# Kernel tuning notes

Hardware: AMD Instinct MI355X
Metric: run time of the kernel (lower is better)

Reference implementation:

```python
import jax, jax.numpy as jnp
import numpy as np

B, N0, N1, FD, L, H = 4, 256, 256, 128, 3, 1
NG = N0 + N1            # nodes per graph
N = B * NG              # total nodes
EPS_BN = 1e-5
EPS_SM = 1e-16


def _build_edges():
    def perm_edges(n, off):
        idx = np.arange(n)
        a = np.repeat(idx, n); b = np.tile(idx, n)
        m = a != b
        return np.stack([a[m], b[m]]) + off
    e_intra = np.concatenate([perm_edges(N0, 0), perm_edges(N1, N0)], axis=1)
    a = np.arange(N0); b = np.arange(N0, N0 + N1)
    cross1 = np.stack([np.repeat(a, N1), np.tile(b, N0)])
    cross2 = np.stack([np.repeat(b, N0), np.tile(a, N1)])
    eg = np.concatenate([e_intra, cross1, cross2], axis=1)
    tg = np.concatenate([np.zeros(e_intra.shape[1], np.int32),
                         np.ones(cross1.shape[1] + cross2.shape[1], np.int32)])
    ei = np.concatenate([eg + g * NG for g in range(B)], axis=1).astype(np.int32)
    et = np.tile(tg, B).astype(np.int32)
    return jnp.asarray(ei), jnp.asarray(et)


def setup_inputs() -> dict:
    key = jax.random.key(0)
    ks = jax.random.split(key, 8)
    edge_index, edge_type = _build_edges()
    return {
        'desc0': jax.random.normal(ks[0], (B, FD, N0), jnp.float32),
        'desc1': jax.random.normal(ks[1], (B, FD, N1), jnp.float32),
        'W': jax.random.normal(ks[2], (L, 2, FD, H * FD), jnp.float32) * (1.0 / np.sqrt(FD)),
        'q': jax.random.normal(ks[3], (L, H * FD, H), jnp.float32) * 0.1,
        'k': jax.random.normal(ks[4], (L, H * FD, H), jnp.float32) * 0.1,
        'conv_b': jnp.zeros((L, FD), jnp.float32),
        'lin_W': jax.random.normal(ks[5], (L, FD, 2 * FD), jnp.float32) * (1.0 / np.sqrt(2 * FD)),
        'lin_b': jnp.zeros((L, FD), jnp.float32),
        'gamma': jnp.ones((L, FD), jnp.float32),
        'beta': jnp.zeros((L, FD), jnp.float32),
        'edge_index': edge_index,
        'edge_type': edge_type,
    }


def _forward(desc0, desc1, W, q, k, conv_b, lin_W, lin_b, gamma, beta, edge_index, edge_type):
    # x: [B, NG, FD] -> flattened batch graph [N, FD]
    x = jnp.concatenate([desc0, desc1], axis=2)        # [B, FD, NG]
    x = jnp.transpose(x, (0, 2, 1)).reshape(N, FD)
    src, dst = edge_index[0], edge_index[1]
    nlayers = W.shape[0]
    heads = q.shape[2]
    for l in range(nlayers):
        # relation-specific node projections (equiv to per-edge bmm with weight[edge_type])
        proj = jnp.einsum('nf,rfo->nro', x, W[l])       # [N, 2, H*FD]
        out_i = proj[dst, edge_type]                    # [E, H*FD]
        out_j = proj[src, edge_type]                    # [E, H*FD]
        alpha = jax.nn.leaky_relu(out_i @ q[l] + out_j @ k[l], 0.2)  # [E, H]
        # softmax over incoming edges of each destination node (across-relation)
        amax = jax.ops.segment_max(alpha, dst, num_segments=N)
        ex = jnp.exp(alpha - amax[dst])
        denom = jax.ops.segment_sum(ex, dst, num_segments=N)
        att = ex / (denom[dst] + EPS_SM)                # [E, H]
        msg = (att[:, :, None] * out_j.reshape(-1, heads, FD)).reshape(-1, heads * FD)
        agg = jax.ops.segment_sum(msg, dst, num_segments=N).reshape(N, heads, FD)
        m1 = jax.nn.relu(agg.mean(axis=1) + conv_b[l])  # concat=False -> mean over heads
        m2 = jnp.concatenate([x, m1], axis=1) @ lin_W[l].T + lin_b[l]
        mu = m2.mean(axis=0)
        var = ((m2 - mu) ** 2).mean(axis=0)             # biased var (BatchNorm training)
        m3 = (m2 - mu) / jnp.sqrt(var + EPS_BN) * gamma[l] + beta[l]
        x = x + m3
    x = x.reshape(B, NG, FD).transpose(0, 2, 1)         # [B, FD, NG]
    return x


def reference(desc0, desc1, W, q, k, conv_b, lin_W, lin_b, gamma, beta, edge_index, edge_type):
    x = _forward(desc0, desc1, W, q, k, conv_b, lin_W, lin_b, gamma, beta, edge_index, edge_type)
    return x[:, :, :N0], x[:, :, N0:]
```

## Files before the change

kernel.cpp:

```cpp
#include <hip/hip_runtime.h>

#define FD  128
#define NN  2048

#define OFF_X     0
#define OFF_QS    262144
#define OFF_KS    266240
#define OFF_SUMS  270336
#define OFF_LWT   276480
#define OFF_M2    374784
#define OFF_QH    636928
#define OFF_KH    637696

__device__ __forceinline__ int swizzle_n0(int bid) {
    int g    = (bid & 7) >> 1;
    int slot = ((bid >> 3) << 1) | (bid & 1);
    return g*512 + slot*4;
}

__device__ __forceinline__ void qsks0(
    const float* __restrict__ W, const float* __restrict__ qv,
    const float* __restrict__ kv, float* __restrict__ ws,
    int n0, int t, const float (*xs)[FD],
    float (*redp)[256], float* red)
{
    int kh = t >> 8, tp = t & 255;
    int rsel = tp >> 7, o = tp & 127;
    const float* Wl = W + ((size_t)rsel*FD)*FD + o;
    float acc[4];
#pragma unroll
    for (int r = 0; r < 4; r++) acc[r] = 0.f;
    int kbase = kh * 64;
#pragma unroll
    for (int kk = 0; kk < 64; kk += 4) {
        int k4 = kbase + kk;
        float w0 = Wl[(k4+0)*FD], w1 = Wl[(k4+1)*FD];
        float w2 = Wl[(k4+2)*FD], w3 = Wl[(k4+3)*FD];
#pragma unroll
        for (int r = 0; r < 4; r++) {
            float4 xq = *(const float4*)&xs[r][k4];
            acc[r] += xq.x*w0 + xq.y*w1 + xq.z*w2 + xq.w*w3;
        }
    }
    if (kh == 1) {
#pragma unroll
        for (int r = 0; r < 4; r++) redp[r][tp] = acc[r];
    }
    __syncthreads();
    if (t < 256) {
#pragma unroll
        for (int r = 0; r < 4; r++) acc[r] += redp[r][tp];
        float qq = qv[o], kq = kv[o];
        int lane = t & 63, w = t >> 6;
#pragma unroll
        for (int r = 0; r < 4; r++) {
            float vq = acc[r]*qq, vk = acc[r]*kq;
            for (int off = 32; off; off >>= 1) {
                vq += __shfl_xor(vq, off, 64);
                vk += __shfl_xor(vk, off, 64);
            }
            if (lane == 0) { red[w*8 + r*2] = vq; red[w*8 + r*2 + 1] = vk; }
        }
    }
    __syncthreads();
    if (t < 16) {
        int r = t & 3, rs = (t >> 2) & 1, wh = t >> 3;
        float v = red[(rs*2)*8 + r*2 + wh] + red[(rs*2 + 1)*8 + r*2 + wh];
        if (wh == 0) ws[OFF_QS + rs*NN + n0 + r] = v;
        else         ws[OFF_KS + rs*NN + n0 + r] = v;
    }
}

__global__ __launch_bounds__(512, 4) void k_pre(
    const float* __restrict__ d0, const float* __restrict__ d1,
    const float* __restrict__ W,  const float* __restrict__ qv,
    const float* __restrict__ kv, const float* __restrict__ linW,
    float* __restrict__ ws)
{
    int bid = blockIdx.x, t = threadIdx.x;
    if (bid >= 512) {
        if (bid < 536) {
            int vb = bid - 512;
#pragma unroll
            for (int i = 0; i < 8; i++) {
                int e = vb*4096 + i*512 + t;
                int l = e >> 15, rem = e & 32767;
                int o = rem >> 8, c = rem & 255;
                ws[OFF_LWT + l*32768 + c*FD + o] = linW[e];
            }
        } else {
            for (int i = t; i < 6144; i += 512) ws[OFF_SUMS + i] = 0.f;
#pragma unroll
            for (int ii = 0; ii < 3; ii++) {
                int e = ii*512 + t;
                int sel = e & 1, idx = e >> 1;
                const float* wrow = W + (size_t)idx*FD;
                int l = idx >> 8;
                const float* vvec = sel ? (kv + l*FD) : (qv + l*FD);
                float acc = 0.f;
                for (int o = 0; o < FD; o++) acc += wrow[o]*vvec[o];
                ws[(sel ? OFF_KH : OFF_QH) + idx] = acc;
            }
        }
        return;
    }
    __shared__ __attribute__((aligned(16))) float xs[4][FD];
    __shared__ float redp[4][256];
    __shared__ float red[32];
    int n0 = swizzle_n0(bid);
    {
        int row = t >> 7, f = t & 127;
        int n = n0 + row, gg = n >> 9, ii = n & 511;
        float v = (ii < 256) ? d0[gg*32768 + f*256 + ii]
                             : d1[gg*32768 + f*256 + (ii - 256)];
        xs[row][f] = v;
        ws[OFF_X + (size_t)n*FD + f] = v;
    }
    __syncthreads();
    qsks0(W, qv, kv, ws, n0, t, xs, redp, red);
}

__global__ __launch_bounds__(512, 4) void k_qs(
    const float* __restrict__ gamma, const float* __restrict__ beta,
    float* __restrict__ ws, int l)
{
    __shared__ float scale[FD], shift[FD];
    __shared__ float red[4][8];
    int bid = blockIdx.x, t = threadIdx.x;
    int lp = l - 1;
    if (t < 128) {
        float s0 = 0.f, s1 = 0.f;
#pragma unroll
        for (int sl = 0; sl < 8; sl++) {
            s0 += ws[OFF_SUMS + lp*2048 + sl*256 + t];
            s1 += ws[OFF_SUMS + lp*2048 + sl*256 + 128 + t];
        }
        float mu  = s0 * (1.f/2048.f);
        float var = s1 * (1.f/2048.f) - mu*mu;
        float rs  = rsqrtf(var + 1e-5f);
        float gm  = gamma[lp*FD + t], bt = beta[lp*FD + t];
        scale[t] = gm * rs;
        shift[t] = bt - mu * gm * rs;
    }
    __syncthreads();
    int n0 = swizzle_n0(bid);
    int row = t >> 7, f = t & 127;
    size_t e = (size_t)(n0 + row)*FD + f;
    float xv = ws[OFF_X + e] + ws[OFF_M2 + e]*scale[f] + shift[f];
    ws[OFF_X + e] = xv;
    float p0 = xv * ws[OFF_QH + l*256 + f];
    float p1 = xv * ws[OFF_QH + l*256 + 128 + f];
    float p2 = xv * ws[OFF_KH + l*256 + f];
    float p3 = xv * ws[OFF_KH + l*256 + 128 + f];
    for (int off = 32; off; off >>= 1) {
        p0 += __shfl_xor(p0, off, 64);
        p1 += __shfl_xor(p1, off, 64);
        p2 += __shfl_xor(p2, off, 64);
        p3 += __shfl_xor(p3, off, 64);
    }
    int lane = t & 63, wh = (t >> 6) & 1;
    if (lane == 0) {
        red[row][wh*4+0] = p0; red[row][wh*4+1] = p1;
        red[row][wh*4+2] = p2; red[row][wh*4+3] = p3;
    }
    __syncthreads();
    if (t < 16) {
        int r = t >> 2, j = t & 3;
        float v = red[r][j] + red[r][4+j];
        int n = n0 + r;
        if      (j == 0) ws[OFF_QS + n] = v;
        else if (j == 1) ws[OFF_QS + NN + n] = v;
        else if (j == 2) ws[OFF_KS + n] = v;
        else             ws[OFF_KS + NN + n] = v;
    }
}

__global__ __launch_bounds__(512, 4) void k_attn(
    const float* __restrict__ Wg,    const float* __restrict__ convb,
    const float* __restrict__ linb,  float* __restrict__ ws, int l)
{
    __shared__ __attribute__((aligned(16))) float att[4*512];
    __shared__ __attribute__((aligned(16))) float redB[8*4*128];
    __shared__ __attribute__((aligned(16))) float hgc[4*256];
    __shared__ float sml[4][2], sls[4][2];
    __shared__ float r1[FD], r2[FD];

    int bid = blockIdx.x, t = threadIdx.x;
    int dstbase = swizzle_n0(bid);
    int g = dstbase >> 9, dloc0 = dstbase & 511;
    int Gd = (dloc0 >= 256) ? 1 : 0;

    {
        int w = t >> 6, p = t & 63;
        int d = w >> 1, h = w & 1;
        int dloc = dloc0 + d;
        float q0 = ws[OFF_QS + dstbase + d];
        float q1 = ws[OFF_QS + NN + dstbase + d];
        float sc[4];
#pragma unroll
        for (int j = 0; j < 4; j++) {
            int s = h*256 + p + j*64;
            int ts = (s < 256) ? Gd : 1 - Gd;
            float a = (ts ? q1 : q0) + ws[OFF_KS + ts*NN + g*512 + s];
            a = a > 0.f ? a : 0.2f*a;
            sc[j] = (s == dloc) ? -1e30f : a;
        }
        float lm = fmaxf(fmaxf(sc[0], sc[1]), fmaxf(sc[2], sc[3]));
        for (int off = 32; off; off >>= 1) lm = fmaxf(lm, __shfl_xor(lm, off, 64));
        float ex[4], lsum = 0.f;
#pragma unroll
        for (int j = 0; j < 4; j++) { ex[j] = __expf(sc[j] - lm); lsum += ex[j]; }
        for (int off = 32; off; off >>= 1) lsum += __shfl_xor(lsum, off, 64);
#pragma unroll
        for (int j = 0; j < 4; j++) att[d*512 + h*256 + p + j*64] = ex[j];
        if (p == 0) { sml[d][h] = lm; sls[d][h] = lsum; }
    }
    __syncthreads();
    {
        int d = t >> 7, s4 = (t & 127) * 4;
        int h = (s4 >= 256) ? 1 : 0;
        float m0 = sml[d][0], m1 = sml[d][1];
        float M = fmaxf(m0, m1);
        float denom = sls[d][0]*__expf(m0 - M) + sls[d][1]*__expf(m1 - M) + 1e-16f;
        float fac = __expf(sml[d][h] - M) / denom;
        float4 a4 = *(float4*)&att[d*512 + s4];
        a4.x *= fac; a4.y *= fac; a4.z *= fac; a4.w *= fac;
        *(float4*)&att[d*512 + s4] = a4;
        if (t < 128) r1[t] = 0.f;
        else if (t < 256) r2[t - 128] = 0.f;
    }
    __syncthreads();

    int f4 = t & 31, sq = t >> 5;
    float acc[4][4];
#pragma unroll
    for (int d2 = 0; d2 < 4; d2++)
#pragma unroll
        for (int j = 0; j < 4; j++) acc[d2][j] = 0.f;
    {
        const float* xp = ws + OFF_X + (size_t)(g*512)*FD + f4*4;
        int s0 = sq * 32;
        float4 bufA[4], bufB[4];
#pragma unroll
        for (int u = 0; u < 4; u++) bufA[u] = *(const float4*)&xp[(size_t)(s0+u)*FD];
#pragma unroll
        for (int ii = 0; ii < 8; ii++) {
            const float4* cur = (ii & 1) ? bufB : bufA;
            float4*       nxt = (ii & 1) ? bufA : bufB;
            if (ii < 7) {
#pragma unroll
                for (int u = 0; u < 4; u++)
                    nxt[u] = *(const float4*)&xp[(size_t)(s0 + (ii+1)*4 + u)*FD];
            }
#pragma unroll
            for (int u = 0; u < 4; u++) {
                int s = s0 + ii*4 + u;
                float4 v = cur[u];
#pragma unroll
                for (int d2 = 0; d2 < 4; d2++) {
                    float b = att[d2*512 + s];
                    acc[d2][0] += b*v.x; acc[d2][1] += b*v.y;
                    acc[d2][2] += b*v.z; acc[d2][3] += b*v.w;
                }
            }
        }
    }
    {
        int slot = (sq & 3) + ((sq >> 3) << 2);
        if (sq & 4) {
#pragma unroll
            for (int d2 = 0; d2 < 4; d2++)
                *(float4*)&redB[(slot*4 + d2)*128 + f4*4] =
                    make_float4(acc[d2][0], acc[d2][1], acc[d2][2], acc[d2][3]);
        }
        __syncthreads();
        if (!(sq & 4)) {
#pragma unroll
            for (int d2 = 0; d2 < 4; d2++) {
                float4 p4 = *(const float4*)&redB[(slot*4 + d2)*128 + f4*4];
                *(float4*)&redB[(slot*4 + d2)*128 + f4*4] =
                    make_float4(acc[d2][0]+p4.x, acc[d2][1]+p4.y, acc[d2][2]+p4.z, acc[d2][3]+p4.w);
            }
        }
        __syncthreads();
    }
    {
        int d2 = t >> 7, f = t & 127;
        float hg0 = redB[(0*4+d2)*128+f] + redB[(1*4+d2)*128+f]
                  + redB[(2*4+d2)*128+f] + redB[(3*4+d2)*128+f];
        float hg1 = redB[(4*4+d2)*128+f] + redB[(5*4+d2)*128+f]
                  + redB[(6*4+d2)*128+f] + redB[(7*4+d2)*128+f];
        hgc[d2*256 + f]       = Gd ? hg1 : hg0;
        hgc[d2*256 + 128 + f] = Gd ? hg0 : hg1;
    }
    __syncthreads();

#pragma unroll
    for (int d2 = 0; d2 < 4; d2++)
#pragma unroll
        for (int j = 0; j < 4; j++) acc[d2][j] = 0.f;
    {
        int rel = sq >> 3;
        const float* wp = Wg + ((size_t)((l*2 + rel)*FD) + (sq & 7)*16)*FD + f4*4;
        int c0 = sq * 16;
        float4 wA[4], wB[4];
#pragma unroll
        for (int u = 0; u < 4; u++) wA[u] = *(const float4*)&wp[(size_t)u*FD];
#pragma unroll
        for (int ii = 0; ii < 4; ii++) {
            const float4* cur = (ii & 1) ? wB : wA;
            float4*       nxt = (ii & 1) ? wA : wB;
            if (ii < 3) {
#pragma unroll
                for (int u = 0; u < 4; u++)
                    nxt[u] = *(const float4*)&wp[(size_t)((ii+1)*4 + u)*FD];
            }
#pragma unroll
            for (int u = 0; u < 4; u++) {
                int c = c0 + ii*4 + u;
                float4 w4 = cur[u];
#pragma unroll
                for (int d2 = 0; d2 < 4; d2++) {
                    float cv = hgc[d2*256 + c];
                    acc[d2][0] += cv*w4.x; acc[d2][1] += cv*w4.y;
                    acc[d2][2] += cv*w4.z; acc[d2][3] += cv*w4.w;
                }
            }
        }
    }
    if (sq >= 8) {
#pragma unroll
        for (int d2 = 0; d2 < 4; d2++)
            *(float4*)&redB[((sq - 8)*4 + d2)*128 + f4*4] =
                make_float4(acc[d2][0], acc[d2][1], acc[d2][2], acc[d2][3]);
    }
    __syncthreads();
    if (sq < 8) {
#pragma unroll
        for (int d2 = 0; d2 < 4; d2++) {
            float4 p4 = *(const float4*)&redB[(sq*4 + d2)*128 + f4*4];
            *(float4*)&redB[(sq*4 + d2)*128 + f4*4] =
                make_float4(acc[d2][0]+p4.x, acc[d2][1]+p4.y, acc[d2][2]+p4.z, acc[d2][3]+p4.w);
        }
    }
    __syncthreads();

    {
        int d2 = t >> 7, f = t & 127;
        float agg = 0.f;
#pragma unroll
        for (int cc = 0; cc < 8; cc++) agg += redB[(cc*4 + d2)*128 + f];
        float m1v = fmaxf(agg + convb[l*FD + f], 0.f);
        hgc[d2*256 + 128 + f] = m1v;
        hgc[d2*256 + f] = ws[OFF_X + (size_t)(dstbase + d2)*FD + f];
    }
    __syncthreads();

#pragma unroll
    for (int d2 = 0; d2 < 4; d2++)
#pragma unroll
        for (int j = 0; j < 4; j++) acc[d2][j] = 0.f;
    {
        const float* lwt = ws + OFF_LWT + l*32768 + f4*4;
        int c0 = sq * 16;
        float4 wA[4], wB[4];
#pragma unroll
        for (int u = 0; u < 4; u++) wA[u] = *(const float4*)&lwt[(c0+u)*128];
#pragma unroll
        for (int ii = 0; ii < 4; ii++) {
            const float4* cur = (ii & 1) ? wB : wA;
            float4*       nxt = (ii & 1) ? wA : wB;
            if (ii < 3) {
#pragma unroll
                for (int u = 0; u < 4; u++)
                    nxt[u] = *(const float4*)&lwt[(c0 + (ii+1)*4 + u)*128];
            }
#pragma unroll
            for (int u = 0; u < 4; u++) {
                int c = c0 + ii*4 + u;
                float4 w4 = cur[u];
#pragma unroll
                for (int d2 = 0; d2 < 4; d2++) {
                    float cv = hgc[d2*256 + c];
                    acc[d2][0] += cv*w4.x; acc[d2][1] += cv*w4.y;
                    acc[d2][2] += cv*w4.z; acc[d2][3] += cv*w4.w;
                }
            }
        }
    }
    if (sq >= 8) {
#pragma unroll
        for (int d2 = 0; d2 < 4; d2++)
            *(float4*)&redB[((sq - 8)*4 + d2)*128 + f4*4] =
                make_float4(acc[d2][0], acc[d2][1], acc[d2][2], acc[d2][3]);
    }
    __syncthreads();
    if (sq < 8) {
#pragma unroll
        for (int d2 = 0; d2 < 4; d2++) {
            float4 p4 = *(const float4*)&redB[(sq*4 + d2)*128 + f4*4];
            *(float4*)&redB[(sq*4 + d2)*128 + f4*4] =
                make_float4(acc[d2][0]+p4.x, acc[d2][1]+p4.y, acc[d2][2]+p4.z, acc[d2][3]+p4.w);
        }
    }
    __syncthreads();

    {
        int d2 = t >> 7, o = t & 127;
        float m2v = linb[l*FD + o];
#pragma unroll
        for (int cc = 0; cc < 8; cc++) m2v += redB[(cc*4 + d2)*128 + o];
        ws[OFF_M2 + (size_t)(dstbase + d2)*FD + o] = m2v;
        atomicAdd(&r1[o], m2v);
        atomicAdd(&r2[o], m2v*m2v);
    }
    __syncthreads();
    if (t < 128) {
        int slot = bid & 7;
        atomicAdd(&ws[OFF_SUMS + l*2048 + slot*256 + t],       r1[t]);
        atomicAdd(&ws[OFF_SUMS + l*2048 + slot*256 + 128 + t], r2[t]);
    }
}

__global__ __launch_bounds__(256) void k_bnout(
    const float* __restrict__ gamma, const float* __restrict__ beta,
    float* __restrict__ ws, float* __restrict__ out)
{
    __shared__ float scale[FD], shift[FD];
    int bid = blockIdx.x, t = threadIdx.x;
    if (t < 128) {
        float s0 = 0.f, s1 = 0.f;
#pragma unroll
        for (int sl = 0; sl < 8; sl++) {
            s0 += ws[OFF_SUMS + 2*2048 + sl*256 + t];
            s1 += ws[OFF_SUMS + 2*2048 + sl*256 + 128 + t];
        }
        float mu  = s0 * (1.f/2048.f);
        float var = s1 * (1.f/2048.f) - mu*mu;
        float rs  = rsqrtf(var + 1e-5f);
        float gm  = gamma[2*FD + t], bt = beta[2*FD + t];
        scale[t] = gm * rs;
        shift[t] = bt - mu * gm * rs;
    }
    __syncthreads();
#pragma unroll
    for (int i = 0; i < 2; i++) {
        int idx = bid*512 + i*256 + t;
        int f = idx & 127, n = idx >> 7;
        float v = ws[OFF_X + idx] + ws[OFF_M2 + idx]*scale[f] + shift[f];
        int gg = n >> 9, ii = n & 511;
        int off = (ii < 256) ? (gg*32768 + f*256 + ii)
                             : (131072 + gg*32768 + f*256 + (ii - 256));
        out[off] = v;
    }
}

extern "C" void kernel_launch(void* const* d_in, const int* in_sizes, int n_in,
                              void* d_out, int out_size, void* d_ws, size_t ws_size,
                              hipStream_t stream) {
    (void)in_sizes; (void)n_in; (void)out_size; (void)ws_size;
    const float* desc0 = (const float*)d_in[0];
    const float* desc1 = (const float*)d_in[1];
    const float* W     = (const float*)d_in[2];
    const float* q     = (const float*)d_in[3];
    const float* kk    = (const float*)d_in[4];
    const float* convb = (const float*)d_in[5];
    const float* linW  = (const float*)d_in[6];
    const float* linb  = (const float*)d_in[7];
    const float* gamma = (const float*)d_in[8];
    const float* beta  = (const float*)d_in[9];
    float* ws  = (float*)d_ws;
    float* out = (float*)d_out;

    hipLaunchKernelGGL(k_pre,  dim3(537), dim3(512), 0, stream, desc0, desc1, W, q, kk, linW, ws);
    hipLaunchKernelGGL(k_attn, dim3(512), dim3(512), 0, stream, W, convb, linb, ws, 0);
    hipLaunchKernelGGL(k_qs,   dim3(512), dim3(512), 0, stream, gamma, beta, ws, 1);
    hipLaunchKernelGGL(k_attn, dim3(512), dim3(512), 0, stream, W, convb, linb, ws, 1);
    hipLaunchKernelGGL(k_qs,   dim3(512), dim3(512), 0, stream, gamma, beta, ws, 2);
    hipLaunchKernelGGL(k_attn, dim3(512), dim3(512), 0, stream, W, convb, linb, ws, 2);
    hipLaunchKernelGGL(k_bnout, dim3(512), dim3(256), 0, stream, gamma, beta, ws, out);
}
```

Baseline: 170.8 us.

## Fuse BatchNorm apply and next-layer q/k projection into attention kernel via grid barrier

Each attention-layer kernel is made a cooperative launch. After it accumulates the BatchNorm sums, a global atomic-counter grid barrier lets every block compute the batch statistics itself, apply normalization and the residual, and either write the next layer's x plus q/k scores or write the final output directly. This removes the separate k_qs and k_bnout launches and the m2 round-trip through global memory. The cost is a spin-wait barrier that relies on all 512 blocks being resident at once, which is checked through an occupancy query, with the old path kept as a fallback.

```diff
diff --git a/kernel.cpp b/kernel.cpp
--- a/kernel.cpp
+++ b/kernel.cpp
@@ -7,10 +7,11 @@
 #define OFF_QS    262144
 #define OFF_KS    266240
 #define OFF_SUMS  270336
-#define OFF_LWT   276480
-#define OFF_M2    374784
-#define OFF_QH    636928
-#define OFF_KH    637696
+#define OFF_CTR   276480
+#define OFF_LWT   276608
+#define OFF_QH    374912
+#define OFF_KH    375680
+#define OFF_M2    376448
 
 __device__ __forceinline__ int swizzle_n0(int bid) {
     int g    = (bid & 7) >> 1;
@@ -89,7 +90,7 @@
                 ws[OFF_LWT + l*32768 + c*FD + o] = linW[e];
             }
         } else {
-            for (int i = t; i < 6144; i += 512) ws[OFF_SUMS + i] = 0.f;
+            for (int i = t; i < 6144 + 128; i += 512) ws[OFF_SUMS + i] = 0.f;
 #pragma unroll
             for (int ii = 0; ii < 3; ii++) {
                 int e = ii*512 + t;
@@ -118,6 +119,326 @@
     }
     __syncthreads();
     qsks0(W, qv, kv, ws, n0, t, xs, redp, red);
+}
+
+template<int MODE>
+__global__ __launch_bounds__(512, 4) void k_attn(
+    const float* __restrict__ Wg,    const float* __restrict__ convb,
+    const float* __restrict__ linb,  const float* __restrict__ gamma,
+    const float* __restrict__ beta,  float* __restrict__ out,
+    float* __restrict__ ws, int l)
+{
+    __shared__ __attribute__((aligned(16))) float att[4*512];
+    __shared__ __attribute__((aligned(16))) float redB[8*4*128];
+    __shared__ __attribute__((aligned(16))) float hgc[4*256];
+    __shared__ float sml[4][2], sls[4][2];
+    __shared__ float r1[FD], r2[FD];
+    __shared__ float sc2[FD], sh2[FD];
+    __shared__ float redq[4][8];
+
+    int bid = blockIdx.x, t = threadIdx.x;
+    int dstbase = swizzle_n0(bid);
+    int g = dstbase >> 9, dloc0 = dstbase & 511;
+    int Gd = (dloc0 >= 256) ? 1 : 0;
+
+    {
+        int w = t >> 6, p = t & 63;
+        int d = w >> 1, h = w & 1;
+        int dloc = dloc0 + d;
+        float q0 = ws[OFF_QS + dstbase + d];
+        float q1 = ws[OFF_QS + NN + dstbase + d];
+        float sc[4];
+#pragma unroll
+        for (int j = 0; j < 4; j++) {
+            int s = h*256 + p + j*64;
+            int ts = (s < 256) ? Gd : 1 - Gd;
+            float a = (ts ? q1 : q0) + ws[OFF_KS + ts*NN + g*512 + s];
+            a = a > 0.f ? a : 0.2f*a;
+            sc[j] = (s == dloc) ? -1e30f : a;
+        }
+        float lm = fmaxf(fmaxf(sc[0], sc[1]), fmaxf(sc[2], sc[3]));
+        for (int off = 32; off; off >>= 1) lm = fmaxf(lm, __shfl_xor(lm, off, 64));
+        float ex[4], lsum = 0.f;
+#pragma unroll
+        for (int j = 0; j < 4; j++) { ex[j] = __expf(sc[j] - lm); lsum += ex[j]; }
+        for (int off = 32; off; off >>= 1) lsum += __shfl_xor(lsum, off, 64);
+#pragma unroll
+        for (int j = 0; j < 4; j++) att[d*512 + h*256 + p + j*64] = ex[j];
+        if (p == 0) { sml[d][h] = lm; sls[d][h] = lsum; }
+    }
+    __syncthreads();
+    {
+        int d = t >> 7, s4 = (t & 127) * 4;
+        int h = (s4 >= 256) ? 1 : 0;
+        float m0 = sml[d][0], m1 = sml[d][1];
+        float M = fmaxf(m0, m1);
+        float denom = sls[d][0]*__expf(m0 - M) + sls[d][1]*__expf(m1 - M) + 1e-16f;
+        float fac = __expf(sml[d][h] - M) / denom;
+        float4 a4 = *(float4*)&att[d*512 + s4];
+        a4.x *= fac; a4.y *= fac; a4.z *= fac; a4.w *= fac;
+        *(float4*)&att[d*512 + s4] = a4;
+        if (t < 128) r1[t] = 0.f;
+        else if (t < 256) r2[t - 128] = 0.f;
+    }
+    __syncthreads();
+
+    int f4 = t & 31, sq = t >> 5;
+    float acc[4][4];
+#pragma unroll
+    for (int d2 = 0; d2 < 4; d2++)
+#pragma unroll
+        for (int j = 0; j < 4; j++) acc[d2][j] = 0.f;
+    {
+        const float* xp = ws + OFF_X + (size_t)(g*512)*FD + f4*4;
+        int s0 = sq * 32;
+        float4 bufA[4], bufB[4];
+#pragma unroll
+        for (int u = 0; u < 4; u++) bufA[u] = *(const float4*)&xp[(size_t)(s0+u)*FD];
+#pragma unroll
+        for (int ii = 0; ii < 8; ii++) {
+            const float4* cur = (ii & 1) ? bufB : bufA;
+            float4*       nxt = (ii & 1) ? bufA : bufB;
+            if (ii < 7) {
+#pragma unroll
+                for (int u = 0; u < 4; u++)
+                    nxt[u] = *(const float4*)&xp[(size_t)(s0 + (ii+1)*4 + u)*FD];
+            }
+#pragma unroll
+            for (int u = 0; u < 4; u++) {
+                int s = s0 + ii*4 + u;
+                float4 v = cur[u];
+#pragma unroll
+                for (int d2 = 0; d2 < 4; d2++) {
+                    float b = att[d2*512 + s];
+                    acc[d2][0] += b*v.x; acc[d2][1] += b*v.y;
+                    acc[d2][2] += b*v.z; acc[d2][3] += b*v.w;
+                }
+            }
+        }
+    }
+    {
+        int slot = (sq & 3) + ((sq >> 3) << 2);
+        if (sq & 4) {
+#pragma unroll
+            for (int d2 = 0; d2 < 4; d2++)
+                *(float4*)&redB[(slot*4 + d2)*128 + f4*4] =
+                    make_float4(acc[d2][0], acc[d2][1], acc[d2][2], acc[d2][3]);
+        }
+        __syncthreads();
+        if (!(sq & 4)) {
+#pragma unroll
+            for (int d2 = 0; d2 < 4; d2++) {
+                float4 p4 = *(const float4*)&redB[(slot*4 + d2)*128 + f4*4];
+                *(float4*)&redB[(slot*4 + d2)*128 + f4*4] =
+                    make_float4(acc[d2][0]+p4.x, acc[d2][1]+p4.y, acc[d2][2]+p4.z, acc[d2][3]+p4.w);
+            }
+        }
+        __syncthreads();
+    }
+    {
+        int d2 = t >> 7, f = t & 127;
+        float hg0 = redB[(0*4+d2)*128+f] + redB[(1*4+d2)*128+f]
+                  + redB[(2*4+d2)*128+f] + redB[(3*4+d2)*128+f];
+        float hg1 = redB[(4*4+d2)*128+f] + redB[(5*4+d2)*128+f]
+                  + redB[(6*4+d2)*128+f] + redB[(7*4+d2)*128+f];
+        hgc[d2*256 + f]       = Gd ? hg1 : hg0;
+        hgc[d2*256 + 128 + f] = Gd ? hg0 : hg1;
+    }
+    __syncthreads();
+
+#pragma unroll
+    for (int d2 = 0; d2 < 4; d2++)
+#pragma unroll
+        for (int j = 0; j < 4; j++) acc[d2][j] = 0.f;
+    {
+        int rel = sq >> 3;
+        const float* wp = Wg + ((size_t)((l*2 + rel)*FD) + (sq & 7)*16)*FD + f4*4;
+        int c0 = sq * 16;
+        float4 wA[4], wB[4];
+#pragma unroll
+        for (int u = 0; u < 4; u++) wA[u] = *(const float4*)&wp[(size_t)u*FD];
+#pragma unroll
+        for (int ii = 0; ii < 4; ii++) {
+            const float4* cur = (ii & 1) ? wB : wA;
+            float4*       nxt = (ii & 1) ? wA : wB;
+            if (ii < 3) {
+#pragma unroll
+                for (int u = 0; u < 4; u++)
+                    nxt[u] = *(const float4*)&wp[(size_t)((ii+1)*4 + u)*FD];
+            }
+#pragma unroll
+            for (int u = 0; u < 4; u++) {
+                int c = c0 + ii*4 + u;
+                float4 w4 = cur[u];
+#pragma unroll
+                for (int d2 = 0; d2 < 4; d2++) {
+                    float cv = hgc[d2*256 + c];
+                    acc[d2][0] += cv*w4.x; acc[d2][1] += cv*w4.y;
+                    acc[d2][2] += cv*w4.z; acc[d2][3] += cv*w4.w;
+                }
+            }
+        }
+    }
+    if (sq >= 8) {
+#pragma unroll
+        for (int d2 = 0; d2 < 4; d2++)
+            *(float4*)&redB[((sq - 8)*4 + d2)*128 + f4*4] =
+                make_float4(acc[d2][0], acc[d2][1], acc[d2][2], acc[d2][3]);
+    }
+    __syncthreads();
+    if (sq < 8) {
+#pragma unroll
+        for (int d2 = 0; d2 < 4; d2++) {
+            float4 p4 = *(const float4*)&redB[(sq*4 + d2)*128 + f4*4];
+            *(float4*)&redB[(sq*4 + d2)*128 + f4*4] =
+                make_float4(acc[d2][0]+p4.x, acc[d2][1]+p4.y, acc[d2][2]+p4.z, acc[d2][3]+p4.w);
+        }
+    }
+    __syncthreads();
+
+    float xold;
+    {
+        int d2 = t >> 7, f = t & 127;
+        float agg = 0.f;
+#pragma unroll
+        for (int cc = 0; cc < 8; cc++) agg += redB[(cc*4 + d2)*128 + f];
+        float m1v = fmaxf(agg + convb[l*FD + f], 0.f);
+        hgc[d2*256 + 128 + f] = m1v;
+        xold = ws[OFF_X + (size_t)(dstbase + d2)*FD + f];
+        hgc[d2*256 + f] = xold;
+    }
+    __syncthreads();
+
+#pragma unroll
+    for (int d2 = 0; d2 < 4; d2++)
+#pragma unroll
+        for (int j = 0; j < 4; j++) acc[d2][j] = 0.f;
+    {
+        const float* lwt = ws + OFF_LWT + l*32768 + f4*4;
+        int c0 = sq * 16;
+        float4 wA[4], wB[4];
+#pragma unroll
+        for (int u = 0; u < 4; u++) wA[u] = *(const float4*)&lwt[(c0+u)*128];
+#pragma unroll
+        for (int ii = 0; ii < 4; ii++) {
+            const float4* cur = (ii & 1) ? wB : wA;
+            float4*       nxt = (ii & 1) ? wA : wB;
+            if (ii < 3) {
+#pragma unroll
+                for (int u = 0; u < 4; u++)
+                    nxt[u] = *(const float4*)&lwt[(c0 + (ii+1)*4 + u)*128];
+            }
+#pragma unroll
+            for (int u = 0; u < 4; u++) {
+                int c = c0 + ii*4 + u;
+                float4 w4 = cur[u];
+#pragma unroll
+                for (int d2 = 0; d2 < 4; d2++) {
+                    float cv = hgc[d2*256 + c];
+                    acc[d2][0] += cv*w4.x; acc[d2][1] += cv*w4.y;
+                    acc[d2][2] += cv*w4.z; acc[d2][3] += cv*w4.w;
+                }
+            }
+        }
+    }
+    if (sq >= 8) {
+#pragma unroll
+        for (int d2 = 0; d2 < 4; d2++)
+            *(float4*)&redB[((sq - 8)*4 + d2)*128 + f4*4] =
+                make_float4(acc[d2][0], acc[d2][1], acc[d2][2], acc[d2][3]);
+    }
+    __syncthreads();
+    if (sq < 8) {
+#pragma unroll
+        for (int d2 = 0; d2 < 4; d2++) {
+            float4 p4 = *(const float4*)&redB[(sq*4 + d2)*128 + f4*4];
+            *(float4*)&redB[(sq*4 + d2)*128 + f4*4] =
+                make_float4(acc[d2][0]+p4.x, acc[d2][1]+p4.y, acc[d2][2]+p4.z, acc[d2][3]+p4.w);
+        }
+    }
+    __syncthreads();
+
+    float m2v;
+    {
+        int d2 = t >> 7, o = t & 127;
+        m2v = linb[l*FD + o];
+#pragma unroll
+        for (int cc = 0; cc < 8; cc++) m2v += redB[(cc*4 + d2)*128 + o];
+        if (MODE == 2) ws[OFF_M2 + (size_t)(dstbase + d2)*FD + o] = m2v;
+        atomicAdd(&r1[o], m2v);
+        atomicAdd(&r2[o], m2v*m2v);
+    }
+    __syncthreads();
+    if (t < 128) {
+        int slot = bid & 7;
+        atomicAdd(&ws[OFF_SUMS + l*2048 + slot*256 + t],       r1[t]);
+        atomicAdd(&ws[OFF_SUMS + l*2048 + slot*256 + 128 + t], r2[t]);
+    }
+    if (MODE == 2) return;
+
+    asm volatile("s_waitcnt vmcnt(0)" ::: "memory");
+    __syncthreads();
+    if (t == 0) {
+        int* ctr = (int*)(ws + OFF_CTR) + l;
+        atomicAdd(ctr, 1);
+        while (atomicAdd(ctr, 0) < 512) __builtin_amdgcn_s_sleep(8);
+    }
+    __syncthreads();
+
+    if (t < 128) {
+        float s0 = 0.f, s1 = 0.f;
+#pragma unroll
+        for (int sl = 0; sl < 8; sl++) {
+            s0 += atomicAdd(&ws[OFF_SUMS + l*2048 + sl*256 + t],       0.f);
+            s1 += atomicAdd(&ws[OFF_SUMS + l*2048 + sl*256 + 128 + t], 0.f);
+        }
+        float mu  = s0 * (1.f/2048.f);
+        float var = s1 * (1.f/2048.f) - mu*mu;
+        float rs  = rsqrtf(var + 1e-5f);
+        float gm  = gamma[l*FD + t], bt = beta[l*FD + t];
+        sc2[t] = gm * rs;
+        sh2[t] = bt - mu * gm * rs;
+    }
+    __syncthreads();
+    {
+        int d2 = t >> 7, o = t & 127;
+        float xnew = xold + m2v*sc2[o] + sh2[o];
+        if (MODE == 0) {
+            ws[OFF_X + (size_t)(dstbase + d2)*FD + o] = xnew;
+            float p0 = xnew * ws[OFF_QH + (l+1)*256 + o];
+            float p1 = xnew * ws[OFF_QH + (l+1)*256 + 128 + o];
+            float p2 = xnew * ws[OFF_KH + (l+1)*256 + o];
+            float p3 = xnew * ws[OFF_KH + (l+1)*256 + 128 + o];
+            for (int off = 32; off; off >>= 1) {
+                p0 += __shfl_xor(p0, off, 64);
+                p1 += __shfl_xor(p1, off, 64);
+                p2 += __shfl_xor(p2, off, 64);
+                p3 += __shfl_xor(p3, off, 64);
+            }
+            int lane = t & 63, wh = (t >> 6) & 1;
+            if (lane == 0) {
+                redq[d2][wh*4+0] = p0; redq[d2][wh*4+1] = p1;
+                redq[d2][wh*4+2] = p2; redq[d2][wh*4+3] = p3;
+            }
+        } else {
+            int n = dstbase + d2, gg = n >> 9, ii = n & 511;
+            int off2 = (ii < 256) ? (gg*32768 + o*256 + ii)
+                                  : (131072 + gg*32768 + o*256 + (ii - 256));
+            out[off2] = xnew;
+        }
+    }
+    if (MODE == 0) {
+        __syncthreads();
+        if (t < 16) {
+            int r = t >> 2, j = t & 3;
+            float v = redq[r][j] + redq[r][4+j];
+            int n = dstbase + r;
+            if      (j == 0) ws[OFF_QS + n] = v;
+            else if (j == 1) ws[OFF_QS + NN + n] = v;
+            else if (j == 2) ws[OFF_KS + n] = v;
+            else             ws[OFF_KS + NN + n] = v;
+        }
+    }
 }
 
 __global__ __launch_bounds__(512, 4) void k_qs(
@@ -172,253 +493,6 @@
         else if (j == 1) ws[OFF_QS + NN + n] = v;
         else if (j == 2) ws[OFF_KS + n] = v;
         else             ws[OFF_KS + NN + n] = v;
-    }
-}
-
-__global__ __launch_bounds__(512, 4) void k_attn(
-    const float* __restrict__ Wg,    const float* __restrict__ convb,
-    const float* __restrict__ linb,  float* __restrict__ ws, int l)
-{
-    __shared__ __attribute__((aligned(16))) float att[4*512];
-    __shared__ __attribute__((aligned(16))) float redB[8*4*128];
-    __shared__ __attribute__((aligned(16))) float hgc[4*256];
-    __shared__ float sml[4][2], sls[4][2];
-    __shared__ float r1[FD], r2[FD];
-
-    int bid = blockIdx.x, t = threadIdx.x;
-    int dstbase = swizzle_n0(bid);
-    int g = dstbase >> 9, dloc0 = dstbase & 511;
-    int Gd = (dloc0 >= 256) ? 1 : 0;
-
-    {
-        int w = t >> 6, p = t & 63;
-        int d = w >> 1, h = w & 1;
-        int dloc = dloc0 + d;
-        float q0 = ws[OFF_QS + dstbase + d];
-        float q1 = ws[OFF_QS + NN + dstbase + d];
-        float sc[4];
-#pragma unroll
-        for (int j = 0; j < 4; j++) {
-            int s = h*256 + p + j*64;
-            int ts = (s < 256) ? Gd : 1 - Gd;
-            float a = (ts ? q1 : q0) + ws[OFF_KS + ts*NN + g*512 + s];
-            a = a > 0.f ? a : 0.2f*a;
-            sc[j] = (s == dloc) ? -1e30f : a;
-        }
-        float lm = fmaxf(fmaxf(sc[0], sc[1]), fmaxf(sc[2], sc[3]));
-        for (int off = 32; off; off >>= 1) lm = fmaxf(lm, __shfl_xor(lm, off, 64));
-        float ex[4], lsum = 0.f;
-#pragma unroll
-        for (int j = 0; j < 4; j++) { ex[j] = __expf(sc[j] - lm); lsum += ex[j]; }
-        for (int off = 32; off; off >>= 1) lsum += __shfl_xor(lsum, off, 64);
-#pragma unroll
-        for (int j = 0; j < 4; j++) att[d*512 + h*256 + p + j*64] = ex[j];
-        if (p == 0) { sml[d][h] = lm; sls[d][h] = lsum; }
-    }
-    __syncthreads();
-    {
-        int d = t >> 7, s4 = (t & 127) * 4;
-        int h = (s4 >= 256) ? 1 : 0;
-        float m0 = sml[d][0], m1 = sml[d][1];
-        float M = fmaxf(m0, m1);
-        float denom = sls[d][0]*__expf(m0 - M) + sls[d][1]*__expf(m1 - M) + 1e-16f;
-        float fac = __expf(sml[d][h] - M) / denom;
-        float4 a4 = *(float4*)&att[d*512 + s4];
-        a4.x *= fac; a4.y *= fac; a4.z *= fac; a4.w *= fac;
-        *(float4*)&att[d*512 + s4] = a4;
-        if (t < 128) r1[t] = 0.f;
-        else if (t < 256) r2[t - 128] = 0.f;
-    }
-    __syncthreads();
-
-    int f4 = t & 31, sq = t >> 5;
-    float acc[4][4];
-#pragma unroll
-    for (int d2 = 0; d2 < 4; d2++)
-#pragma unroll
-        for (int j = 0; j < 4; j++) acc[d2][j] = 0.f;
-    {
-        const float* xp = ws + OFF_X + (size_t)(g*512)*FD + f4*4;
-        int s0 = sq * 32;
-        float4 bufA[4], bufB[4];
-#pragma unroll
-        for (int u = 0; u < 4; u++) bufA[u] = *(const float4*)&xp[(size_t)(s0+u)*FD];
-#pragma unroll
-        for (int ii = 0; ii < 8; ii++) {
-            const float4* cur = (ii & 1) ? bufB : bufA;
-            float4*       nxt = (ii & 1) ? bufA : bufB;
-            if (ii < 7) {
-#pragma unroll
-                for (int u = 0; u < 4; u++)
-                    nxt[u] = *(const float4*)&xp[(size_t)(s0 + (ii+1)*4 + u)*FD];
-            }
-#pragma unroll
-            for (int u = 0; u < 4; u++) {
-                int s = s0 + ii*4 + u;
-                float4 v = cur[u];
-#pragma unroll
-                for (int d2 = 0; d2 < 4; d2++) {
-                    float b = att[d2*512 + s];
-                    acc[d2][0] += b*v.x; acc[d2][1] += b*v.y;
-                    acc[d2][2] += b*v.z; acc[d2][3] += b*v.w;
-                }
-            }
-        }
-    }
-    {
-        int slot = (sq & 3) + ((sq >> 3) << 2);
-        if (sq & 4) {
-#pragma unroll
-            for (int d2 = 0; d2 < 4; d2++)
-                *(float4*)&redB[(slot*4 + d2)*128 + f4*4] =
-                    make_float4(acc[d2][0], acc[d2][1], acc[d2][2], acc[d2][3]);
-        }
-        __syncthreads();
-        if (!(sq & 4)) {
-#pragma unroll
-            for (int d2 = 0; d2 < 4; d2++) {
-                float4 p4 = *(const float4*)&redB[(slot*4 + d2)*128 + f4*4];
-                *(float4*)&redB[(slot*4 + d2)*128 + f4*4] =
-                    make_float4(acc[d2][0]+p4.x, acc[d2][1]+p4.y, acc[d2][2]+p4.z, acc[d2][3]+p4.w);
-            }
-        }
-        __syncthreads();
-    }
-    {
-        int d2 = t >> 7, f = t & 127;
-        float hg0 = redB[(0*4+d2)*128+f] + redB[(1*4+d2)*128+f]
-                  + redB[(2*4+d2)*128+f] + redB[(3*4+d2)*128+f];
-        float hg1 = redB[(4*4+d2)*128+f] + redB[(5*4+d2)*128+f]
-                  + redB[(6*4+d2)*128+f] + redB[(7*4+d2)*128+f];
-        hgc[d2*256 + f]       = Gd ? hg1 : hg0;
-        hgc[d2*256 + 128 + f] = Gd ? hg0 : hg1;
-    }
-    __syncthreads();
-
-#pragma unroll
-    for (int d2 = 0; d2 < 4; d2++)
-#pragma unroll
-        for (int j = 0; j < 4; j++) acc[d2][j] = 0.f;
-    {
-        int rel = sq >> 3;
-        const float* wp = Wg + ((size_t)((l*2 + rel)*FD) + (sq & 7)*16)*FD + f4*4;
-        int c0 = sq * 16;
-        float4 wA[4], wB[4];
-#pragma unroll
-        for (int u = 0; u < 4; u++) wA[u] = *(const float4*)&wp[(size_t)u*FD];
-#pragma unroll
-        for (int ii = 0; ii < 4; ii++) {
-            const float4* cur = (ii & 1) ? wB : wA;
-            float4*       nxt = (ii & 1) ? wA : wB;
-            if (ii < 3) {
-#pragma unroll
-                for (int u = 0; u < 4; u++)
-                    nxt[u] = *(const float4*)&wp[(size_t)((ii+1)*4 + u)*FD];
-            }
-#pragma unroll
-            for (int u = 0; u < 4; u++) {
-                int c = c0 + ii*4 + u;
-                float4 w4 = cur[u];
-#pragma unroll
-                for (int d2 = 0; d2 < 4; d2++) {
-                    float cv = hgc[d2*256 + c];
-                    acc[d2][0] += cv*w4.x; acc[d2][1] += cv*w4.y;
-                    acc[d2][2] += cv*w4.z; acc[d2][3] += cv*w4.w;
-                }
-            }
-        }
-    }
-    if (sq >= 8) {
-#pragma unroll
-        for (int d2 = 0; d2 < 4; d2++)
-            *(float4*)&redB[((sq - 8)*4 + d2)*128 + f4*4] =
-                make_float4(acc[d2][0], acc[d2][1], acc[d2][2], acc[d2][3]);
-    }
-    __syncthreads();
-    if (sq < 8) {
-#pragma unroll
-        for (int d2 = 0; d2 < 4; d2++) {
-            float4 p4 = *(const float4*)&redB[(sq*4 + d2)*128 + f4*4];
-            *(float4*)&redB[(sq*4 + d2)*128 + f4*4] =
-                make_float4(acc[d2][0]+p4.x, acc[d2][1]+p4.y, acc[d2][2]+p4.z, acc[d2][3]+p4.w);
-        }
-    }
-    __syncthreads();
-
-    {
-        int d2 = t >> 7, f = t & 127;
-        float agg = 0.f;
-#pragma unroll
-        for (int cc = 0; cc < 8; cc++) agg += redB[(cc*4 + d2)*128 + f];
-        float m1v = fmaxf(agg + convb[l*FD + f], 0.f);
-        hgc[d2*256 + 128 + f] = m1v;
-        hgc[d2*256 + f] = ws[OFF_X + (size_t)(dstbase + d2)*FD + f];
-    }
-    __syncthreads();
-
-#pragma unroll
-    for (int d2 = 0; d2 < 4; d2++)
-#pragma unroll
-        for (int j = 0; j < 4; j++) acc[d2][j] = 0.f;
-    {
-        const float* lwt = ws + OFF_LWT + l*32768 + f4*4;
-        int c0 = sq * 16;
-        float4 wA[4], wB[4];
-#pragma unroll
-        for (int u = 0; u < 4; u++) wA[u] = *(const float4*)&lwt[(c0+u)*128];
-#pragma unroll
-        for (int ii = 0; ii < 4; ii++) {
-            const float4* cur = (ii & 1) ? wB : wA;
-            float4*       nxt = (ii & 1) ? wA : wB;
-            if (ii < 3) {
-#pragma unroll
-                for (int u = 0; u < 4; u++)
-                    nxt[u] = *(const float4*)&lwt[(c0 + (ii+1)*4 + u)*128];
-            }
-#pragma unroll
-            for (int u = 0; u < 4; u++) {
-                int c = c0 + ii*4 + u;
-                float4 w4 = cur[u];
-#pragma unroll
-                for (int d2 = 0; d2 < 4; d2++) {
-                    float cv = hgc[d2*256 + c];
-                    acc[d2][0] += cv*w4.x; acc[d2][1] += cv*w4.y;
-                    acc[d2][2] += cv*w4.z; acc[d2][3] += cv*w4.w;
-                }
-            }
-        }
-    }
-    if (sq >= 8) {
-#pragma unroll
-        for (int d2 = 0; d2 < 4; d2++)
-            *(float4*)&redB[((sq - 8)*4 + d2)*128 + f4*4] =
-                make_float4(acc[d2][0], acc[d2][1], acc[d2][2], acc[d2][3]);
-    }
-    __syncthreads();
-    if (sq < 8) {
-#pragma unroll
-        for (int d2 = 0; d2 < 4; d2++) {
-            float4 p4 = *(const float4*)&redB[(sq*4 + d2)*128 + f4*4];
-            *(float4*)&redB[(sq*4 + d2)*128 + f4*4] =
-                make_float4(acc[d2][0]+p4.x, acc[d2][1]+p4.y, acc[d2][2]+p4.z, acc[d2][3]+p4.w);
-        }
-    }
-    __syncthreads();
-
-    {
-        int d2 = t >> 7, o = t & 127;
-        float m2v = linb[l*FD + o];
-#pragma unroll
-        for (int cc = 0; cc < 8; cc++) m2v += redB[(cc*4 + d2)*128 + o];
-        ws[OFF_M2 + (size_t)(dstbase + d2)*FD + o] = m2v;
-        atomicAdd(&r1[o], m2v);
-        atomicAdd(&r2[o], m2v*m2v);
-    }
-    __syncthreads();
-    if (t < 128) {
-        int slot = bid & 7;
-        atomicAdd(&ws[OFF_SUMS + l*2048 + slot*256 + t],       r1[t]);
-        atomicAdd(&ws[OFF_SUMS + l*2048 + slot*256 + 128 + t], r2[t]);
     }
 }
 
@@ -472,11 +546,45 @@
     float* ws  = (float*)d_ws;
     float* out = (float*)d_out;
 
-    hipLaunchKernelGGL(k_pre,  dim3(537), dim3(512), 0, stream, desc0, desc1, W, q, kk, linW, ws);
-    hipLaunchKernelGGL(k_attn, dim3(512), dim3(512), 0, stream, W, convb, linb, ws, 0);
-    hipLaunchKernelGGL(k_qs,   dim3(512), dim3(512), 0, stream, gamma, beta, ws, 1);
-    hipLaunchKernelGGL(k_attn, dim3(512), dim3(512), 0, stream, W, convb, linb, ws, 1);
-    hipLaunchKernelGGL(k_qs,   dim3(512), dim3(512), 0, stream, gamma, beta, ws, 2);
-    hipLaunchKernelGGL(k_attn, dim3(512), dim3(512), 0, stream, W, convb, linb, ws, 2);
-    hipLaunchKernelGGL(k_bnout, dim3(512), dim3(256), 0, stream, gamma, beta, ws, out);
-}
+    static int g_fused = -1;
+    if (g_fused < 0) {
+        int nb = 0, ncu = 0, dev = 0;
+        hipError_t e1 = hipOccupancyMaxActiveBlocksPerMultiprocessor(
+            &nb, reinterpret_cast<const void*>(&k_attn<0>), 512, 0);
+        hipDeviceProp_t prop;
+        if (hipGetDevice(&dev) == hipSuccess &&
+            hipGetDeviceProperties(&prop, dev) == hipSuccess)
+            ncu = prop.multiProcessorCount;
+        g_fused = (e1 == hipSuccess && nb > 0 && ncu > 0 && nb * ncu >= 512) ? 1 : 0;
+    }
+
+    hipLaunchKernelGGL(k_pre, dim3(537), dim3(512), 0, stream,
+                       desc0, desc1, W, q, kk, linW, ws);
+
+    if (g_fused) {
+        static int Ls[3] = {0, 1, 2};
+        void* a0[] = {(void*)&W, (void*)&convb, (void*)&linb, (void*)&gamma,
+                      (void*)&beta, (void*)&out, (void*)&ws, (void*)&Ls[0]};
+        void* a1[] = {(void*)&W, (void*)&convb, (void*)&linb, (void*)&gamma,
+                      (void*)&beta, (void*)&out, (void*)&ws, (void*)&Ls[1]};
+        void* a2[] = {(void*)&W, (void*)&convb, (void*)&linb, (void*)&gamma,
+                      (void*)&beta, (void*)&out, (void*)&ws, (void*)&Ls[2]};
+        hipLaunchCooperativeKernel(reinterpret_cast<const void*>(&k_attn<0>),
+                                   dim3(512), dim3(512), a0, 0, stream);
+        hipLaunchCooperativeKernel(reinterpret_cast<const void*>(&k_attn<0>),
+                                   dim3(512), dim3(512), a1, 0, stream);
+        hipLaunchCooperativeKernel(reinterpret_cast<const void*>(&k_attn<1>),
+                                   dim3(512), dim3(512), a2, 0, stream);
+    } else {
+        hipLaunchKernelGGL((k_attn<2>), dim3(512), dim3(512), 0, stream,
+                           W, convb, linb, gamma, beta, out, ws, 0);
+        hipLaunchKernelGGL(k_qs, dim3(512), dim3(512), 0, stream, gamma, beta, ws, 1);
+        hipLaunchKernelGGL((k_attn<2>), dim3(512), dim3(512), 0, stream,
+                           W, convb, linb, gamma, beta, out, ws, 1);
+        hipLaunchKernelGGL(k_qs, dim3(512), dim3(512), 0, stream, gamma, beta, ws, 2);
+        hipLaunchKernelGGL((k_attn<2>), dim3(512), dim3(512), 0, stream,
+                           W, convb, linb, gamma, beta, out, ws, 2);
+        hipLaunchKernelGGL(k_bnout, dim3(512), dim3(256), 0, stream,
+                           gamma, beta, ws, out);
+    }
+}
```

New measurement: 172.8 us. Within noise of the previous version (+1.2%).
